# Performance work log

Measured on AMD Instinct MI355X. Metric: run time of the kernel, lower is better.

## Reference

```python
import jax, jax.numpy as jnp
import numpy as np

DIM = 1024

def setup_inputs() -> dict:
    key = jax.random.key(0)
    ks = jax.random.split(key, 7)
    s = 1.0 / np.sqrt(DIM)
    x = jax.random.normal(ks[0], (8, 2048, DIM), dtype=jnp.float32)
    Wq = jax.random.uniform(ks[1], (DIM, DIM), jnp.float32, -s, s)
    bq = jax.random.uniform(ks[2], (DIM,), jnp.float32, -s, s)
    Wk = jax.random.uniform(ks[3], (DIM, DIM), jnp.float32, -s, s)
    bk = jax.random.uniform(ks[4], (DIM,), jnp.float32, -s, s)
    Wv = jax.random.uniform(ks[5], (DIM, DIM), jnp.float32, -s, s)
    bv = jax.random.uniform(ks[6], (DIM,), jnp.float32, -s, s)
    return {"x": x, "Wq": Wq, "bq": bq, "Wk": Wk, "bk": bk, "Wv": Wv, "bv": bv}

def reference(x, Wq, bq, Wk, bk, Wv, bv):
    # x: [B, S, D]; torch Linear: x @ W.T + b (W here stored transposed: [D_in, D_out])
    scale = x.shape[-1] ** (-0.5)
    q = x @ Wq + bq                      # [B, S, D]
    k = x @ Wk + bk
    v = x @ Wv + bv
    scores = jnp.einsum('bsd,btd->bst', q, k) * scale  # [B, S, S]
    attn = jax.nn.softmax(scores, axis=-1)
    out = jnp.einsum('bst,btd->bsd', attn, v)          # [B, S, D]
    return out.mean(axis=1)                            # [B, D]
```

## Files before the change

### kernel.cpp

```cpp
#include <hip/hip_runtime.h>


using bf16x8 = __attribute__((ext_vector_type(8))) __bf16;
using u16x8  = __attribute__((ext_vector_type(8))) unsigned short;
using f32x4  = __attribute__((ext_vector_type(4))) float;
using f32x2  = __attribute__((ext_vector_type(2))) float;

#define NB 8
#define SEQ 2048
#define DIM 1024
#define MTOT (NB * SEQ)

__device__ __forceinline__ unsigned short f2bf(float f) {
    unsigned int u = __float_as_uint(f);
    u = u + 0x7FFFu + ((u >> 16) & 1u);
    return (unsigned short)(u >> 16);
}
__device__ __forceinline__ float bf2f(unsigned short h) {
    return __uint_as_float(((unsigned int)h) << 16);
}

__device__ __forceinline__ void async16(const unsigned short* g, unsigned short* l) {
    __builtin_amdgcn_global_load_lds(
        (const __attribute__((address_space(1))) void*)g,
        (__attribute__((address_space(3))) void*)l, 16, 0, 0);
}
__device__ __forceinline__ void async16b(const unsigned char* g, unsigned char* l) {
    __builtin_amdgcn_global_load_lds(
        (const __attribute__((address_space(1))) void*)g,
        (__attribute__((address_space(3))) void*)l, 16, 0, 0);
}

__global__ __launch_bounds__(256) void k_prep(const float* __restrict__ Wk,
                                              const float* __restrict__ Wq,
                                              const float* __restrict__ bq,
                                              const float* __restrict__ bv,
                                              unsigned short* __restrict__ wkb,
                                              unsigned short* __restrict__ wqb,
                                              float* __restrict__ u,
                                              float* __restrict__ out) {
    const int bid = blockIdx.x;
    if (bid < 2048) {
        const float* src = (bid >= 1024) ? Wq : Wk;
        unsigned short* dst = (bid >= 1024) ? wqb : wkb;
        size_t i = ((size_t)(bid & 1023) * 256 + threadIdx.x) * 4;
        float4 v = *reinterpret_cast<const float4*>(src + i);
        ushort4 o;
        o.x = f2bf(v.x); o.y = f2bf(v.y); o.z = f2bf(v.z); o.w = f2bf(v.w);
        *reinterpret_cast<ushort4*>(dst + i) = o;
    } else if (bid < 2304) {
        const int wave = threadIdx.x >> 6, lane = threadIdx.x & 63;
        const int row = (bid - 2048) * 4 + wave;
        const float* wr = Wk + (size_t)row * DIM;
        float s = 0.f;
#pragma unroll
        for (int p = 0; p < 4; ++p) {
            int col = p * 256 + lane * 4;
            float4 v = *reinterpret_cast<const float4*>(wr + col);
            float4 b = *reinterpret_cast<const float4*>(bq + col);
            s += v.x * b.x + v.y * b.y + v.z * b.z + v.w * b.w;
        }
#pragma unroll
        for (int off = 32; off; off >>= 1) s += __shfl_xor(s, off);
        if (lane == 0) u[row] = s;
    } else {
        int i = (bid - 2304) * 256 + threadIdx.x;
        out[i] = bv[i & (DIM - 1)];
    }
}

__global__ __launch_bounds__(256) void k_cvt_x(const float* __restrict__ x,
                                               const float* __restrict__ u,
                                               unsigned short* __restrict__ xb,
                                               unsigned char* __restrict__ xb8,
                                               float* __restrict__ c) {
    __shared__ float red[4];
    const int row = blockIdx.x, tid = threadIdx.x;
    size_t i = (size_t)row * DIM + tid * 4;
    float4 v = *reinterpret_cast<const float4*>(x + i);
    ushort4 o;
    o.x = f2bf(v.x); o.y = f2bf(v.y); o.z = f2bf(v.z); o.w = f2bf(v.w);
    *reinterpret_cast<ushort4*>(xb + i) = o;
    int pk = __builtin_amdgcn_cvt_pk_fp8_f32(v.x, v.y, 0, false);
    pk = __builtin_amdgcn_cvt_pk_fp8_f32(v.z, v.w, pk, true);
    *reinterpret_cast<unsigned int*>(xb8 + i) = (unsigned int)pk;
    float4 uv = *reinterpret_cast<const float4*>(u + tid * 4);
    float s = v.x * uv.x + v.y * uv.y + v.z * uv.z + v.w * uv.w;
#pragma unroll
    for (int off = 32; off; off >>= 1) s += __shfl_xor(s, off);
    if ((tid & 63) == 0) red[tid >> 6] = s;
    __syncthreads();
    if (tid == 0) c[row] = 0.03125f * (red[0] + red[1] + red[2] + red[3]);
}

__device__ __forceinline__ void gemm_bt_tile128(const unsigned short* __restrict__ A,
                                                const unsigned short* __restrict__ Bt,
                                                int K, int m0, int n0, int lda, int ldb,
                                                unsigned short* ldsA, unsigned short* ldsB,
                                                f32x4 acc[4][4]) {
    const int tid  = threadIdx.x;
    const int wave = tid >> 6;
    const int lane = tid & 63;
    const int lrow = lane >> 3;
    const int lcol = lane & 7;
    const int wm = (wave >> 1) * 64;
    const int wn = (wave & 1) * 64;
    const int fr = lane & 15;
    const int fg = lane >> 4;

    for (int k0 = 0; k0 < K; k0 += 64) {
#pragma unroll
        for (int r = 0; r < 4; ++r) {
            int row = r * 32 + wave * 8 + lrow;
            async16(A + (size_t)(m0 + row) * lda + k0 + lcol * 8, ldsA + r * 2048 + wave * 512);
            async16(Bt + (size_t)(n0 + row) * ldb + k0 + lcol * 8, ldsB + r * 2048 + wave * 512);
        }
        __syncthreads();
#pragma unroll
        for (int ks = 0; ks < 2; ++ks) {
            bf16x8 af[4], bfr[4];
#pragma unroll
            for (int mf = 0; mf < 4; ++mf)
                af[mf] = *reinterpret_cast<const bf16x8*>(ldsA + (wm + mf * 16 + fr) * 64 + ks * 32 + fg * 8);
#pragma unroll
            for (int nf = 0; nf < 4; ++nf)
                bfr[nf] = *reinterpret_cast<const bf16x8*>(ldsB + (wn + nf * 16 + fr) * 64 + ks * 32 + fg * 8);
#pragma unroll
            for (int mf = 0; mf < 4; ++mf)
#pragma unroll
                for (int nf = 0; nf < 4; ++nf)
                    acc[mf][nf] = __builtin_amdgcn_mfma_f32_16x16x32_bf16(af[mf], bfr[nf], acc[mf][nf], 0, 0, 0);
        }
        __syncthreads();
    }
}

__global__ __launch_bounds__(256) void k_mm(const unsigned short* __restrict__ wkb,
                                            const unsigned short* __restrict__ wqb,
                                            unsigned char* __restrict__ Mt8) {
    __shared__ unsigned short ldsA[128 * 64];
    __shared__ unsigned short ldsB[128 * 64];
    int m0 = blockIdx.x * 128, n0 = blockIdx.y * 128;
    f32x4 acc[4][4] = {};
    gemm_bt_tile128(wkb, wqb, DIM, m0, n0, DIM, DIM, ldsA, ldsB, acc);
    const int lane = threadIdx.x & 63, wave = threadIdx.x >> 6;
    const int wm = (wave >> 1) * 64, wn = (wave & 1) * 64;
    const int fr = lane & 15, fg = lane >> 4;
#pragma unroll
    for (int nf = 0; nf < 4; ++nf) {
        int n = n0 + wn + nf * 16 + fr;
#pragma unroll
        for (int mf = 0; mf < 4; ++mf) {
            int r0 = m0 + wm + mf * 16 + fg * 4;
            int pk01 = __builtin_amdgcn_cvt_pk_fp8_f32(acc[mf][nf][0] * 64.f, acc[mf][nf][1] * 64.f, 0, false);
            int pk23 = __builtin_amdgcn_cvt_pk_fp8_f32(acc[mf][nf][2] * 64.f, acc[mf][nf][3] * 64.f, 0, false);
            Mt8[(size_t)(r0 + 0) * DIM + n] = (unsigned char)(pk01 & 0xff);
            Mt8[(size_t)(r0 + 1) * DIM + n] = (unsigned char)((pk01 >> 8) & 0xff);
            Mt8[(size_t)(r0 + 2) * DIM + n] = (unsigned char)(pk23 & 0xff);
            Mt8[(size_t)(r0 + 3) * DIM + n] = (unsigned char)((pk23 >> 8) & 0xff);
        }
    }
}


#define STAGE8(gbase, ld, dstoff)                                         \
    do {                                                                  \
        async16b((gbase), ldsb + (dstoff));                               \
        async16b((gbase) + 8 * (size_t)(ld), ldsb + (dstoff) + 1024);     \
    } while (0)
#define STAGE8_A(buf, half, kt) STAGE8(gA + (size_t)((half) * 128) * lda + (kt) * 128, lda, (buf) * 32768 + (half) * 16384)
#define STAGE8_B(buf, half, kt) STAGE8(gB + (size_t)((half) * 128) * ldb + (kt) * 128, ldb, 65536 + (buf) * 32768 + (half) * 16384)

#define FRAG8(base_b, row, colb) \
    (*reinterpret_cast<const long*>(ldsb + (base_b) + (row) * 128 + ((colb) ^ (((row) & 7) << 4))))

#define READ8_A(dbuf, mh)                                                     \
    _Pragma("unroll") for (int m2 = 0; m2 < 4; ++m2) {                        \
        int arow = ((mh) * 4 + m2) * 16 + fr;                                 \
        _Pragma("unroll") for (int ks = 0; ks < 4; ++ks)                      \
            afc[(mh) * 4 + m2][ks] =                                          \
                FRAG8((dbuf) * 32768 + wr * 16384, arow, ks * 32 + fg * 8);   \
    }
#define READ8_B(dbuf, nh)                                                     \
    _Pragma("unroll") for (int n2 = 0; n2 < 2; ++n2) {                        \
        int brow = (wc & 1) * 64 + ((nh) * 2 + n2) * 16 + fr;                 \
        _Pragma("unroll") for (int ks = 0; ks < 4; ++ks)                      \
            bfc[nh][n2][ks] =                                                 \
                FRAG8(65536 + (dbuf) * 32768 + (wc >> 1) * 16384, brow,       \
                      ks * 32 + fg * 8);                                      \
    }

#define VM4 asm volatile("s_waitcnt vmcnt(4)" ::: "memory")

#define PHASE8(mh, nh, STG, VM, PF)                                           \
    do {                                                                      \
        STG;                                                                  \
        VM;                                                                   \
        asm volatile("s_barrier" ::: "memory");                               \
        asm volatile("s_waitcnt lgkmcnt(0)" ::: "memory");                    \
        __builtin_amdgcn_sched_barrier(0);                                    \
        PF;                                                                   \
        __builtin_amdgcn_sched_barrier(0);                                    \
        __builtin_amdgcn_s_setprio(1);                                        \
        _Pragma("unroll") for (int m2 = 0; m2 < 4; ++m2)                      \
        _Pragma("unroll") for (int n2 = 0; n2 < 2; ++n2)                      \
        _Pragma("unroll") for (int ks = 0; ks < 4; ++ks)                      \
            acc[(mh) * 4 + m2][(nh) * 2 + n2] =                               \
                __builtin_amdgcn_mfma_f32_16x16x32_fp8_fp8(                   \
                    afc[(mh) * 4 + m2][ks], bfc[nh][n2][ks],                  \
                    acc[(mh) * 4 + m2][(nh) * 2 + n2], 0, 0, 0);              \
        __builtin_amdgcn_s_setprio(0);                                        \
    } while (0)

__device__ __forceinline__ void gemm256_fp8(const unsigned char* __restrict__ A,
                                            const unsigned char* __restrict__ Bt,
                                            int lda, int ldb, int m0, int n0,
                                            unsigned char* ldsb, f32x4 (&acc)[8][4]) {
    constexpr int NKT = 1024 / 128;
    constexpr int NIT = NKT / 2;
    const int tid = threadIdx.x;
    const int w = tid >> 6, lane = tid & 63;
    const int wr = w >> 2, wc = w & 3;
    const int fr = lane & 15, fg = lane >> 4;
    const int r8 = lane >> 3, slot = (lane & 7) ^ r8;

    const unsigned char* gA = A + (size_t)(m0 + w * 16 + r8) * lda + slot * 16;
    const unsigned char* gB = Bt + (size_t)(n0 + w * 16 + r8) * ldb + slot * 16;
    unsigned char* ldsbw = ldsb + w * 2048;
    #define ldsb ldsbw_alias
    unsigned char* ldsbw_alias = ldsbw;
    #undef ldsb

    long afc[8][4];
    long bfc[2][2][4];

    {
        unsigned char* ldsb = ldsbw;
        STAGE8_A(0, 0, 0); STAGE8_A(0, 1, 0); STAGE8_B(0, 0, 0); STAGE8_B(0, 1, 0);
        STAGE8_A(1, 0, 1); STAGE8_A(1, 1, 1);
    }
    VM4;
    asm volatile("s_barrier" ::: "memory");
    {
        unsigned char* ldsb = ldsbw - w * 2048;
        READ8_A(0, 0); READ8_B(0, 0);
    }

    unsigned char* ldsb_rd = ldsbw - w * 2048;
    for (int it = 0; it < NIT; ++it) {
        const int t1 = 2 * it + 1;
        const int ka = (2 * it + 2) & (NKT - 1);
        const int kb = (2 * it + 3) & (NKT - 1);
        unsigned char* ldsb = ldsbw;
        {
            #define RD_LDS unsigned char* ldsb = ldsb_rd;
            PHASE8(0, 0, STAGE8_B(1, 0, t1), , { RD_LDS READ8_A(0, 1); });
            PHASE8(1, 0, STAGE8_B(1, 1, t1), , { RD_LDS READ8_B(0, 1); });
            PHASE8(0, 1, STAGE8_A(0, 0, ka), , );
            PHASE8(1, 1, STAGE8_A(0, 1, ka), VM4, { RD_LDS READ8_A(1, 0); READ8_B(1, 0); });
            PHASE8(0, 0, STAGE8_B(0, 0, ka), , { RD_LDS READ8_A(1, 1); });
            PHASE8(1, 0, STAGE8_B(0, 1, ka), , { RD_LDS READ8_B(1, 1); });
            PHASE8(0, 1, STAGE8_A(1, 0, kb), , );
            PHASE8(1, 1, STAGE8_A(1, 1, kb), VM4, { RD_LDS READ8_A(0, 0); READ8_B(0, 0); });
            #undef RD_LDS
        }
    }
    asm volatile("s_waitcnt vmcnt(0) lgkmcnt(0)" ::: "memory");
}

__global__ __launch_bounds__(512, 2) void k_proj_y(const unsigned char* __restrict__ xb8,
                                                   const unsigned char* __restrict__ Mt8,
                                                   unsigned char* __restrict__ y8) {
    __shared__ unsigned char lds[131072];
    const int f = blockIdx.x;
    const int m_hi = f & 7, j = f >> 3;
    const int n_t = j & 3, m_lo = j >> 2;
    const int m0 = (m_hi * 8 + m_lo) * 256, n0 = n_t * 256;

    f32x4 acc[8][4] = {};
    gemm256_fp8(xb8, Mt8, DIM, DIM, m0, n0, lds, acc);

    const int tid = threadIdx.x, w = tid >> 6, lane = tid & 63;
    const int wr = w >> 2, wc = w & 3, fr = lane & 15, fg = lane >> 4;
#pragma unroll
    for (int nf = 0; nf < 4; ++nf) {
        int n = n0 + wc * 64 + nf * 16 + fr;
#pragma unroll
        for (int mf = 0; mf < 8; ++mf) {
            int r0 = m0 + wr * 128 + mf * 16 + fg * 4;
            int pk01 = __builtin_amdgcn_cvt_pk_fp8_f32(acc[mf][nf][0] * 0.125f, acc[mf][nf][1] * 0.125f, 0, false);
            int pk23 = __builtin_amdgcn_cvt_pk_fp8_f32(acc[mf][nf][2] * 0.125f, acc[mf][nf][3] * 0.125f, 0, false);
            y8[(size_t)(r0 + 0) * DIM + n] = (unsigned char)(pk01 & 0xff);
            y8[(size_t)(r0 + 1) * DIM + n] = (unsigned char)((pk01 >> 8) & 0xff);
            y8[(size_t)(r0 + 2) * DIM + n] = (unsigned char)(pk23 & 0xff);
            y8[(size_t)(r0 + 3) * DIM + n] = (unsigned char)((pk23 >> 8) & 0xff);
        }
    }
}

__global__ __launch_bounds__(512, 2) void k_scores(const unsigned char* __restrict__ y8,
                                                   const unsigned char* __restrict__ xb8,
                                                   const float* __restrict__ c,
                                                   unsigned char* __restrict__ PT,
                                                   float* __restrict__ ell) {
    __shared__ unsigned char lds[131072];
    const int f = blockIdx.x;
    const int b = f & 7, j = f >> 3;
    const int mt = j & 7, nt = j >> 3;
    const unsigned char* q = y8 + (size_t)b * SEQ * DIM;
    const unsigned char* k = xb8 + (size_t)b * SEQ * DIM;
    const int m0 = mt * 256, n0 = nt * 256;

    f32x4 acc[8][4] = {};
    gemm256_fp8(q, k, DIM, DIM, m0, n0, lds, acc);

    const float scl8 = 0.00390625f;
    const int tid = threadIdx.x, w = tid >> 6, lane = tid & 63;
    const int wr = w >> 2, wc = w & 3, fr = lane & 15, fg = lane >> 4;
    unsigned char* Pb = PT + (size_t)b * SEQ * SEQ;
    float cv[4];
#pragma unroll
    for (int nf = 0; nf < 4; ++nf)
        cv[nf] = c[(size_t)b * SEQ + n0 + wc * 64 + nf * 16 + fr];
#pragma unroll
    for (int mf = 0; mf < 8; ++mf) {
        const int sbase = m0 + wr * 128 + mf * 16 + fg * 4;
        float rs[4] = {0.f, 0.f, 0.f, 0.f};
#pragma unroll
        for (int nf = 0; nf < 4; ++nf) {
            int t = n0 + wc * 64 + nf * 16 + fr;
            float p0 = __expf(fmaf(acc[mf][nf][0], scl8, cv[nf]));
            float p1 = __expf(fmaf(acc[mf][nf][1], scl8, cv[nf]));
            float p2 = __expf(fmaf(acc[mf][nf][2], scl8, cv[nf]));
            float p3 = __expf(fmaf(acc[mf][nf][3], scl8, cv[nf]));
            int pk = __builtin_amdgcn_cvt_pk_fp8_f32(p0, p1, 0, false);
            pk = __builtin_amdgcn_cvt_pk_fp8_f32(p2, p3, pk, true);
            *reinterpret_cast<unsigned int*>(Pb + (size_t)t * SEQ + sbase) = (unsigned int)pk;
            f32x2 d01 = __builtin_amdgcn_cvt_pk_f32_fp8(pk, false);
            f32x2 d23 = __builtin_amdgcn_cvt_pk_f32_fp8(pk, true);
            rs[0] += d01[0]; rs[1] += d01[1]; rs[2] += d23[0]; rs[3] += d23[1];
        }
#pragma unroll
        for (int j2 = 0; j2 < 4; ++j2) {
            float r = rs[j2];
            r += __shfl_xor(r, 1);
            r += __shfl_xor(r, 2);
            r += __shfl_xor(r, 4);
            r += __shfl_xor(r, 8);
            if (fr == 0) atomicAdd(&ell[b * SEQ + sbase + j2], r);
        }
    }
}

__global__ __launch_bounds__(256) void k_colsum(const unsigned char* __restrict__ PT,
                                                const float* __restrict__ ell,
                                                float* __restrict__ w) {
    __shared__ float rel[512];
    const int b = blockIdx.z;
    const int s0 = blockIdx.x * 512;
    const int t = blockIdx.y * 256 + threadIdx.x;
    {
        int i = threadIdx.x;
        rel[i]       = 1.0f / ell[b * SEQ + s0 + i];
        rel[i + 256] = 1.0f / ell[b * SEQ + s0 + 256 + i];
    }
    __syncthreads();
    const unsigned char* Pt = PT + (size_t)b * SEQ * SEQ + (size_t)t * SEQ + s0;
    float a = 0.f;
    for (int i = 0; i < 512; i += 8) {
        uint2 pv = *reinterpret_cast<const uint2*>(Pt + i);
        f32x2 d0 = __builtin_amdgcn_cvt_pk_f32_fp8((int)pv.x, false);
        f32x2 d1 = __builtin_amdgcn_cvt_pk_f32_fp8((int)pv.x, true);
        f32x2 d2 = __builtin_amdgcn_cvt_pk_f32_fp8((int)pv.y, false);
        f32x2 d3 = __builtin_amdgcn_cvt_pk_f32_fp8((int)pv.y, true);
        a += d0[0] * rel[i]     + d0[1] * rel[i + 1] + d1[0] * rel[i + 2] + d1[1] * rel[i + 3];
        a += d2[0] * rel[i + 4] + d2[1] * rel[i + 5] + d3[0] * rel[i + 6] + d3[1] * rel[i + 7];
    }
    atomicAdd(&w[b * SEQ + t], a);
}

__global__ __launch_bounds__(256) void k_accx(const float* __restrict__ w,
                                              const unsigned short* __restrict__ xb,
                                              float* __restrict__ g) {
    const int b = blockIdx.y;
    const int t0 = blockIdx.x * 64 + (threadIdx.x >> 7) * 32;
    const int d8 = (threadIdx.x & 127) * 8;
    const unsigned short* xbb = xb + (size_t)b * SEQ * DIM;
    const float* wb = w + b * SEQ;
    float a[8] = {};
    for (int i = 0; i < 32; ++i) {
        int t = t0 + i;
        float wt = wb[t];
        u16x8 v = *reinterpret_cast<const u16x8*>(xbb + (size_t)t * DIM + d8);
#pragma unroll
        for (int j = 0; j < 8; ++j) a[j] += wt * bf2f(v[j]);
    }
#pragma unroll
    for (int j = 0; j < 8; ++j)
        atomicAdd(&g[b * DIM + d8 + j], a[j] * (1.0f / (float)SEQ));
}

__global__ __launch_bounds__(256) void k_out2(const float* __restrict__ g,
                                              const float* __restrict__ Wv,
                                              float* __restrict__ out) {
    int b = blockIdx.y;
    int n = blockIdx.x * 256 + threadIdx.x;
    int d0 = blockIdx.z * 64;
    const float* gb = g + b * DIM;
    float acc = 0.f;
#pragma unroll
    for (int d = 0; d < 64; ++d)
        acc += gb[d0 + d] * Wv[(size_t)(d0 + d) * DIM + n];
    atomicAdd(&out[b * DIM + n], acc);
}

extern "C" void kernel_launch(void* const* d_in, const int* in_sizes, int n_in,
                              void* d_out, int out_size, void* d_ws, size_t ws_size,
                              hipStream_t stream) {
    const float* x  = (const float*)d_in[0];
    const float* Wq = (const float*)d_in[1];
    const float* bq = (const float*)d_in[2];
    const float* Wk = (const float*)d_in[3];
    const float* bk = (const float*)d_in[4];
    const float* Wv = (const float*)d_in[5];
    const float* bv = (const float*)d_in[6];
    float* out = (float*)d_out;
    (void)bk;

    char* ws = (char*)d_ws;
    unsigned short* xb  = (unsigned short*)(ws);
    unsigned short* wkb = (unsigned short*)(ws + 33554432ull);
    unsigned short* wqb = (unsigned short*)(ws + 35651584ull);
    unsigned char*  Mt8 = (unsigned char*)(ws + 37748736ull);
    unsigned char*  xb8 = (unsigned char*)(ws + 38797312ull);
    unsigned char*  y8  = (unsigned char*)(ws + 55574528ull);
    unsigned char*  PT  = (unsigned char*)(ws + 72351744ull);
    float*          ell = (float*)(ws + 105906176ull);
    float*          w   = (float*)(ws + 105971712ull);
    float*          g   = (float*)(ws + 106037248ull);
    float*          c   = (float*)(ws + 106070016ull);
    float*          u   = (float*)(ws + 106135552ull);

    hipMemsetAsync(ell, 0, 163840, stream);

    k_prep<<<dim3(2336), 256, 0, stream>>>(Wk, Wq, bq, bv, wkb, wqb, u, out);
    k_cvt_x<<<dim3(MTOT), 256, 0, stream>>>(x, u, xb, xb8, c);
    k_mm<<<dim3(8, 8), 256, 0, stream>>>(wkb, wqb, Mt8);
    k_proj_y<<<dim3(256), 512, 0, stream>>>(xb8, Mt8, y8);
    k_scores<<<dim3(512), 512, 0, stream>>>(y8, xb8, c, PT, ell);
    k_colsum<<<dim3(SEQ / 512, SEQ / 256, NB), 256, 0, stream>>>(PT, ell, w);
    k_accx<<<dim3(SEQ / 64, NB), 256, 0, stream>>>(w, xb, g);
    k_out2<<<dim3(DIM / 256, NB, 16), 256, 0, stream>>>(g, Wv, out);
}
```

Baseline: 214.1 us.

## Permute fp8 K-dimension layout so MFMA fragments load as 16-byte LDS reads

Writes xb8, Mt8 and y8 with a within-128 column permutation. Each lane's four 8-byte k-slices become contiguous, so the fp8 GEMM fragments can be read from LDS as two 16-byte loads instead of four 8-byte loads. This halves the number of LDS read instructions in the inner loop. The contraction result is unchanged because both operands share the same permutation. The cost is scattered byte writes and a permuted layout that every consumer of these buffers must agree on.

Result: faster. 189.7 us (-11.4%).

```diff
diff --git a/kernel.cpp b/kernel.cpp
--- a/kernel.cpp
+++ b/kernel.cpp
@@ -5,6 +5,7 @@
 using u16x8  = __attribute__((ext_vector_type(8))) unsigned short;
 using f32x4  = __attribute__((ext_vector_type(4))) float;
 using f32x2  = __attribute__((ext_vector_type(2))) float;
+using i64x2  = __attribute__((ext_vector_type(2))) long;
 
 #define NB 8
 #define SEQ 2048
@@ -19,6 +20,9 @@
 __device__ __forceinline__ float bf2f(unsigned short h) {
     return __uint_as_float(((unsigned int)h) << 16);
 }
+__device__ __forceinline__ int perm128(int n) {
+    return (n & ~127) + ((n >> 3) & 3) * 32 + ((n & 127) >> 5) * 8 + (n & 7);
+}
 
 __device__ __forceinline__ void async16(const unsigned short* g, unsigned short* l) {
     __builtin_amdgcn_global_load_lds(
@@ -29,6 +33,9 @@
     __builtin_amdgcn_global_load_lds(
         (const __attribute__((address_space(1))) void*)g,
         (__attribute__((address_space(3))) void*)l, 16, 0, 0);
+}
+__device__ __forceinline__ f32x4 mfma8(long a, long b, f32x4 c) {
+    return __builtin_amdgcn_mfma_f32_16x16x32_fp8_fp8(a, b, c, 0, 0, 0);
 }
 
 __global__ __launch_bounds__(256) void k_prep(const float* __restrict__ Wk,
@@ -83,7 +90,8 @@
     *reinterpret_cast<ushort4*>(xb + i) = o;
     int pk = __builtin_amdgcn_cvt_pk_fp8_f32(v.x, v.y, 0, false);
     pk = __builtin_amdgcn_cvt_pk_fp8_f32(v.z, v.w, pk, true);
-    *reinterpret_cast<unsigned int*>(xb8 + i) = (unsigned int)pk;
+    int pp = perm128(tid * 4);
+    *reinterpret_cast<unsigned int*>(xb8 + (size_t)row * DIM + pp) = (unsigned int)pk;
     float4 uv = *reinterpret_cast<const float4*>(u + tid * 4);
     float s = v.x * uv.x + v.y * uv.y + v.z * uv.z + v.w * uv.w;
 #pragma unroll
@@ -149,15 +157,16 @@
 #pragma unroll
     for (int nf = 0; nf < 4; ++nf) {
         int n = n0 + wn + nf * 16 + fr;
+        int pn = perm128(n);
 #pragma unroll
         for (int mf = 0; mf < 4; ++mf) {
             int r0 = m0 + wm + mf * 16 + fg * 4;
             int pk01 = __builtin_amdgcn_cvt_pk_fp8_f32(acc[mf][nf][0] * 64.f, acc[mf][nf][1] * 64.f, 0, false);
             int pk23 = __builtin_amdgcn_cvt_pk_fp8_f32(acc[mf][nf][2] * 64.f, acc[mf][nf][3] * 64.f, 0, false);
-            Mt8[(size_t)(r0 + 0) * DIM + n] = (unsigned char)(pk01 & 0xff);
-            Mt8[(size_t)(r0 + 1) * DIM + n] = (unsigned char)((pk01 >> 8) & 0xff);
-            Mt8[(size_t)(r0 + 2) * DIM + n] = (unsigned char)(pk23 & 0xff);
-            Mt8[(size_t)(r0 + 3) * DIM + n] = (unsigned char)((pk23 >> 8) & 0xff);
+            Mt8[(size_t)(r0 + 0) * DIM + pn] = (unsigned char)(pk01 & 0xff);
+            Mt8[(size_t)(r0 + 1) * DIM + pn] = (unsigned char)((pk01 >> 8) & 0xff);
+            Mt8[(size_t)(r0 + 2) * DIM + pn] = (unsigned char)(pk23 & 0xff);
+            Mt8[(size_t)(r0 + 3) * DIM + pn] = (unsigned char)((pk23 >> 8) & 0xff);
         }
     }
 }
@@ -165,29 +174,29 @@
 
 #define STAGE8(gbase, ld, dstoff)                                         \
     do {                                                                  \
-        async16b((gbase), ldsb + (dstoff));                               \
-        async16b((gbase) + 8 * (size_t)(ld), ldsb + (dstoff) + 1024);     \
+        async16b((gbase), ldsw + (dstoff));                               \
+        async16b((gbase) + 8 * (size_t)(ld), ldsw + (dstoff) + 1024);     \
     } while (0)
 #define STAGE8_A(buf, half, kt) STAGE8(gA + (size_t)((half) * 128) * lda + (kt) * 128, lda, (buf) * 32768 + (half) * 16384)
 #define STAGE8_B(buf, half, kt) STAGE8(gB + (size_t)((half) * 128) * ldb + (kt) * 128, ldb, 65536 + (buf) * 32768 + (half) * 16384)
 
 #define FRAG8(base_b, row, colb) \
-    (*reinterpret_cast<const long*>(ldsb + (base_b) + (row) * 128 + ((colb) ^ (((row) & 7) << 4))))
+    (*reinterpret_cast<const i64x2*>(lds + (base_b) + (row) * 128 + ((colb) ^ (((row) & 7) << 4))))
 
 #define READ8_A(dbuf, mh)                                                     \
     _Pragma("unroll") for (int m2 = 0; m2 < 4; ++m2) {                        \
         int arow = ((mh) * 4 + m2) * 16 + fr;                                 \
-        _Pragma("unroll") for (int ks = 0; ks < 4; ++ks)                      \
-            afc[(mh) * 4 + m2][ks] =                                          \
-                FRAG8((dbuf) * 32768 + wr * 16384, arow, ks * 32 + fg * 8);   \
+        _Pragma("unroll") for (int h = 0; h < 2; ++h)                         \
+            afc[(mh) * 4 + m2][h] =                                           \
+                FRAG8((dbuf) * 32768 + wr * 16384, arow, fg * 32 + h * 16);   \
     }
 #define READ8_B(dbuf, nh)                                                     \
     _Pragma("unroll") for (int n2 = 0; n2 < 2; ++n2) {                        \
         int brow = (wc & 1) * 64 + ((nh) * 2 + n2) * 16 + fr;                 \
-        _Pragma("unroll") for (int ks = 0; ks < 4; ++ks)                      \
-            bfc[nh][n2][ks] =                                                 \
+        _Pragma("unroll") for (int h = 0; h < 2; ++h)                         \
+            bfc[nh][n2][h] =                                                  \
                 FRAG8(65536 + (dbuf) * 32768 + (wc >> 1) * 16384, brow,       \
-                      ks * 32 + fg * 8);                                      \
+                      fg * 32 + h * 16);                                      \
     }
 
 #define VM4 asm volatile("s_waitcnt vmcnt(4)" ::: "memory")
@@ -203,19 +212,20 @@
         __builtin_amdgcn_sched_barrier(0);                                    \
         __builtin_amdgcn_s_setprio(1);                                        \
         _Pragma("unroll") for (int m2 = 0; m2 < 4; ++m2)                      \
-        _Pragma("unroll") for (int n2 = 0; n2 < 2; ++n2)                      \
-        _Pragma("unroll") for (int ks = 0; ks < 4; ++ks)                      \
-            acc[(mh) * 4 + m2][(nh) * 2 + n2] =                               \
-                __builtin_amdgcn_mfma_f32_16x16x32_fp8_fp8(                   \
-                    afc[(mh) * 4 + m2][ks], bfc[nh][n2][ks],                  \
-                    acc[(mh) * 4 + m2][(nh) * 2 + n2], 0, 0, 0);              \
+        _Pragma("unroll") for (int n2 = 0; n2 < 2; ++n2) {                    \
+            f32x4& a = acc[(mh) * 4 + m2][(nh) * 2 + n2];                     \
+            a = mfma8(afc[(mh) * 4 + m2][0][0], bfc[nh][n2][0][0], a);        \
+            a = mfma8(afc[(mh) * 4 + m2][0][1], bfc[nh][n2][0][1], a);        \
+            a = mfma8(afc[(mh) * 4 + m2][1][0], bfc[nh][n2][1][0], a);        \
+            a = mfma8(afc[(mh) * 4 + m2][1][1], bfc[nh][n2][1][1], a);        \
+        }                                                                     \
         __builtin_amdgcn_s_setprio(0);                                        \
     } while (0)
 
 __device__ __forceinline__ void gemm256_fp8(const unsigned char* __restrict__ A,
                                             const unsigned char* __restrict__ Bt,
                                             int lda, int ldb, int m0, int n0,
-                                            unsigned char* ldsb, f32x4 (&acc)[8][4]) {
+                                            unsigned char* lds, f32x4 (&acc)[8][4]) {
     constexpr int NKT = 1024 / 128;
     constexpr int NIT = NKT / 2;
     const int tid = threadIdx.x;
@@ -226,44 +236,29 @@
 
     const unsigned char* gA = A + (size_t)(m0 + w * 16 + r8) * lda + slot * 16;
     const unsigned char* gB = Bt + (size_t)(n0 + w * 16 + r8) * ldb + slot * 16;
-    unsigned char* ldsbw = ldsb + w * 2048;
-    #define ldsb ldsbw_alias
-    unsigned char* ldsbw_alias = ldsbw;
-    #undef ldsb
-
-    long afc[8][4];
-    long bfc[2][2][4];
-
-    {
-        unsigned char* ldsb = ldsbw;
-        STAGE8_A(0, 0, 0); STAGE8_A(0, 1, 0); STAGE8_B(0, 0, 0); STAGE8_B(0, 1, 0);
-        STAGE8_A(1, 0, 1); STAGE8_A(1, 1, 1);
-    }
+    unsigned char* ldsw = lds + w * 2048;
+
+    i64x2 afc[8][2];
+    i64x2 bfc[2][2][2];
+
+    STAGE8_A(0, 0, 0); STAGE8_A(0, 1, 0); STAGE8_B(0, 0, 0); STAGE8_B(0, 1, 0);
+    STAGE8_A(1, 0, 1); STAGE8_A(1, 1, 1);
     VM4;
     asm volatile("s_barrier" ::: "memory");
-    {
-        unsigned char* ldsb = ldsbw - w * 2048;
-        READ8_A(0, 0); READ8_B(0, 0);
-    }
-
-    unsigned char* ldsb_rd = ldsbw - w * 2048;
+    READ8_A(0, 0); READ8_B(0, 0);
+
     for (int it = 0; it < NIT; ++it) {
         const int t1 = 2 * it + 1;
         const int ka = (2 * it + 2) & (NKT - 1);
         const int kb = (2 * it + 3) & (NKT - 1);
-        unsigned char* ldsb = ldsbw;
-        {
-            #define RD_LDS unsigned char* ldsb = ldsb_rd;
-            PHASE8(0, 0, STAGE8_B(1, 0, t1), , { RD_LDS READ8_A(0, 1); });
-            PHASE8(1, 0, STAGE8_B(1, 1, t1), , { RD_LDS READ8_B(0, 1); });
-            PHASE8(0, 1, STAGE8_A(0, 0, ka), , );
-            PHASE8(1, 1, STAGE8_A(0, 1, ka), VM4, { RD_LDS READ8_A(1, 0); READ8_B(1, 0); });
-            PHASE8(0, 0, STAGE8_B(0, 0, ka), , { RD_LDS READ8_A(1, 1); });
-            PHASE8(1, 0, STAGE8_B(0, 1, ka), , { RD_LDS READ8_B(1, 1); });
-            PHASE8(0, 1, STAGE8_A(1, 0, kb), , );
-            PHASE8(1, 1, STAGE8_A(1, 1, kb), VM4, { RD_LDS READ8_A(0, 0); READ8_B(0, 0); });
-            #undef RD_LDS
-        }
+        PHASE8(0, 0, STAGE8_B(1, 0, t1), , READ8_A(0, 1));
+        PHASE8(1, 0, STAGE8_B(1, 1, t1), , READ8_B(0, 1));
+        PHASE8(0, 1, STAGE8_A(0, 0, ka), , );
+        PHASE8(1, 1, STAGE8_A(0, 1, ka), VM4, READ8_A(1, 0); READ8_B(1, 0));
+        PHASE8(0, 0, STAGE8_B(0, 0, ka), , READ8_A(1, 1));
+        PHASE8(1, 0, STAGE8_B(0, 1, ka), , READ8_B(1, 1));
+        PHASE8(0, 1, STAGE8_A(1, 0, kb), , );
+        PHASE8(1, 1, STAGE8_A(1, 1, kb), VM4, READ8_A(0, 0); READ8_B(0, 0));
     }
     asm volatile("s_waitcnt vmcnt(0) lgkmcnt(0)" ::: "memory");
 }
@@ -285,15 +280,16 @@
 #pragma unroll
     for (int nf = 0; nf < 4; ++nf) {
         int n = n0 + wc * 64 + nf * 16 + fr;
+        int pn = perm128(n);
 #pragma unroll
         for (int mf = 0; mf < 8; ++mf) {
             int r0 = m0 + wr * 128 + mf * 16 + fg * 4;
             int pk01 = __builtin_amdgcn_cvt_pk_fp8_f32(acc[mf][nf][0] * 0.125f, acc[mf][nf][1] * 0.125f, 0, false);
             int pk23 = __builtin_amdgcn_cvt_pk_fp8_f32(acc[mf][nf][2] * 0.125f, acc[mf][nf][3] * 0.125f, 0, false);
-            y8[(size_t)(r0 + 0) * DIM + n] = (unsigned char)(pk01 & 0xff);
-            y8[(size_t)(r0 + 1) * DIM + n] = (unsigned char)((pk01 >> 8) & 0xff);
-            y8[(size_t)(r0 + 2) * DIM + n] = (unsigned char)(pk23 & 0xff);
-            y8[(size_t)(r0 + 3) * DIM + n] = (unsigned char)((pk23 >> 8) & 0xff);
+            y8[(size_t)(r0 + 0) * DIM + pn] = (unsigned char)(pk01 & 0xff);
+            y8[(size_t)(r0 + 1) * DIM + pn] = (unsigned char)((pk01 >> 8) & 0xff);
+            y8[(size_t)(r0 + 2) * DIM + pn] = (unsigned char)(pk23 & 0xff);
+            y8[(size_t)(r0 + 3) * DIM + pn] = (unsigned char)((pk23 >> 8) & 0xff);
         }
     }
 }
```
